# Performance work log

Measured on AMD Instinct MI355X. Metric: run time of the kernel, lower is better.

Reference implementation:

```python
import jax, jax.numpy as jnp
import numpy as np

Q_DIM = 1024
CTX_DIM = 1024
HEADS = 16
DIM_HEAD = 64
INNER = HEADS * DIM_HEAD  # 1024
MLP_HIDDEN = int(4.0 * Q_DIM)
EPS = 1e-5


def layer_norm(x, g, b):
    mu = jnp.mean(x, axis=-1, keepdims=True)
    var = jnp.var(x, axis=-1, keepdims=True)
    return (x - mu) * jax.lax.rsqrt(var + EPS) * g + b


def setup_inputs() -> dict:
    key = jax.random.key(0)
    ks = jax.random.split(key, 12)
    s = 0.02
    return {
        "x": jax.random.normal(ks[0], (4, 2048, Q_DIM), jnp.float32),
        "context": jax.random.normal(ks[1], (4, 2048, CTX_DIM), jnp.float32),
        # attention projections (stored [in, out])
        "Wq": jax.random.normal(ks[2], (Q_DIM, INNER), jnp.float32) * s,
        "Wk": jax.random.normal(ks[3], (CTX_DIM, INNER), jnp.float32) * s,
        "Wv": jax.random.normal(ks[4], (CTX_DIM, INNER), jnp.float32) * s,
        "Wo": jax.random.normal(ks[5], (INNER, Q_DIM), jnp.float32) * s,
        "bo": jnp.zeros((Q_DIM,), jnp.float32),
        # layer norms
        "g_q": jnp.ones((Q_DIM,), jnp.float32), "b_q": jnp.zeros((Q_DIM,), jnp.float32),
        "g_k": jnp.ones((CTX_DIM,), jnp.float32), "b_k": jnp.zeros((CTX_DIM,), jnp.float32),
        "g_m": jnp.ones((Q_DIM,), jnp.float32), "b_m": jnp.zeros((Q_DIM,), jnp.float32),
        # mlp
        "W1": jax.random.normal(ks[6], (Q_DIM, MLP_HIDDEN), jnp.float32) * s,
        "b1": jnp.zeros((MLP_HIDDEN,), jnp.float32),
        "W2": jax.random.normal(ks[7], (MLP_HIDDEN, Q_DIM), jnp.float32) * s,
        "b2": jnp.zeros((Q_DIM,), jnp.float32),
    }


def reference(x, context, Wq, Wk, Wv, Wo, bo, g_q, b_q, g_k, b_k, g_m, b_m, W1, b1, W2, b2):
    B, N, _ = x.shape
    M = context.shape[1]
    scale = DIM_HEAD ** -0.5

    xn = layer_norm(x, g_q, b_q)
    cn = layer_norm(context, g_k, b_k)

    # project and split heads: [B, H, N, D]
    q = (xn @ Wq).reshape(B, N, HEADS, DIM_HEAD).transpose(0, 2, 1, 3)
    k = (cn @ Wk).reshape(B, M, HEADS, DIM_HEAD).transpose(0, 2, 1, 3)
    v = (cn @ Wv).reshape(B, M, HEADS, DIM_HEAD).transpose(0, 2, 1, 3)

    sim = jnp.einsum('bhid,bhjd->bhij', q, k) * scale  # [B,H,N,M]
    attn = jax.nn.softmax(sim, axis=-1)
    out = jnp.einsum('bhij,bhjd->bhid', attn, v)        # [B,H,N,D]
    out = out.transpose(0, 2, 1, 3).reshape(B, N, INNER)
    x = x + out @ Wo + bo

    h = layer_norm(x, g_m, b_m)
    h = jax.nn.silu(h @ W1 + b1) @ W2 + b2
    return x + h
```

## Files before the change

kernel.cpp:

```cpp
#include <hip/hip_runtime.h>
#include <hip/hip_bf16.h>


typedef __bf16 bf16x8 __attribute__((ext_vector_type(8)));
typedef __bf16 bf16x4 __attribute__((ext_vector_type(4)));
typedef float f32x4 __attribute__((ext_vector_type(4)));

#define DEV static __device__ __forceinline__

DEV short f2bf(float x) {
  union { float f; unsigned u; } c; c.f = x;
  unsigned r = c.u + 0x7fffu + ((c.u >> 16) & 1u);
  return (short)(r >> 16);
}

DEV void gload_lds16(const void* g, void* l) {
  __builtin_amdgcn_global_load_lds((__attribute__((address_space(1))) void*)g,
                                   (__attribute__((address_space(3))) void*)l, 16, 0, 0);
}

__launch_bounds__(256, 4)
__global__ void transpose_f32_bf16(const float* __restrict__ in, short* __restrict__ outT,
                                   int R, int C) {
  __shared__ float t[32][33];
  const int c0 = blockIdx.x * 32, r0 = blockIdx.y * 32;
  const int tx = threadIdx.x, ty = threadIdx.y;
#pragma unroll
  for (int i = 0; i < 4; ++i)
    t[ty + 8 * i][tx] = in[(size_t)(r0 + ty + 8 * i) * C + (c0 + tx)];
  __syncthreads();
#pragma unroll
  for (int i = 0; i < 4; ++i)
    outT[(size_t)(c0 + ty + 8 * i) * R + (r0 + tx)] = f2bf(t[tx][ty + 8 * i]);
}

__launch_bounds__(256, 4)
__global__ void transpose_v(const short* __restrict__ V, short* __restrict__ Vt) {
  __shared__ short t[32][33];
  const int m0 = blockIdx.x * 32;
  const int d0 = blockIdx.y * 32;
  const int bh = blockIdx.z;
  const int b = bh >> 4, h = bh & 15;
  const int tx = threadIdx.x, ty = threadIdx.y;
#pragma unroll
  for (int i = 0; i < 4; ++i)
    t[ty + 8 * i][tx] = V[((size_t)b * 2048 + m0 + ty + 8 * i) * 1024 + h * 64 + d0 + tx];
  __syncthreads();
#pragma unroll
  for (int i = 0; i < 4; ++i)
    Vt[((size_t)bh * 64 + d0 + ty + 8 * i) * 2048 + (m0 + tx)] = t[tx][ty + 8 * i];
}

__launch_bounds__(256, 4)
__global__ void ln_kernel(const float* __restrict__ in, const float* __restrict__ g,
                          const float* __restrict__ b, short* __restrict__ out) {
  const int row = blockIdx.x;
  const int tid = threadIdx.x;
  const float4 v = ((const float4*)(in + (size_t)row * 1024))[tid];
  float s = v.x + v.y + v.z + v.w;
  float s2 = v.x * v.x + v.y * v.y + v.z * v.z + v.w * v.w;
#pragma unroll
  for (int off = 1; off < 64; off <<= 1) {
    s += __shfl_xor(s, off);
    s2 += __shfl_xor(s2, off);
  }
  __shared__ float ps[4], pq[4];
  const int w = tid >> 6, lane = tid & 63;
  if (lane == 0) { ps[w] = s; pq[w] = s2; }
  __syncthreads();
  s = ps[0] + ps[1] + ps[2] + ps[3];
  s2 = pq[0] + pq[1] + pq[2] + pq[3];
  const float mu = s * (1.f / 1024.f);
  const float rs = rsqrtf(s2 * (1.f / 1024.f) - mu * mu + 1e-5f);
  const float4 gg = ((const float4*)g)[tid];
  const float4 bb = ((const float4*)b)[tid];
  short4 o4;
  o4.x = f2bf((v.x - mu) * rs * gg.x + bb.x);
  o4.y = f2bf((v.y - mu) * rs * gg.y + bb.y);
  o4.z = f2bf((v.z - mu) * rs * gg.z + bb.z);
  o4.w = f2bf((v.w - mu) * rs * gg.w + bb.w);
  ((short4*)(out + (size_t)row * 1024))[tid] = o4;
}

enum { EPI_Q = 0, EPI_PLAIN = 1, EPI_BIAS_RESID_F32 = 2, EPI_BIAS_SILU = 3 };

template <int EPI>
__launch_bounds__(256, 2)
__global__ void gemm_bt(const short* __restrict__ A, const short* __restrict__ Bt,
                        int N, int K, const float* __restrict__ bias,
                        const float* __restrict__ resid, float scale,
                        short* __restrict__ outb, float* __restrict__ outf) {
  __shared__ short Al[128 * 64];
  __shared__ short Bl[128 * 64];
  const int tid = threadIdx.x;
  const int lane = tid & 63, w = tid >> 6;
  const int wrow = w >> 1, wcol = w & 1;
  const int lg = lane >> 4, lr = lane & 15;
  const int row0 = blockIdx.y * 128, col0 = blockIdx.x * 128;

  f32x4 acc[4][4] = {};

  const int sr = w * 32 + (lane >> 3);
  const int scb = ((lane & 7) * 16) ^ (((lane >> 3) & 7) << 4);
  const int fswz = (lr & 7) << 4;

  for (int kk = 0; kk < K; kk += 64) {
    __syncthreads();
#pragma unroll
    for (int i = 0; i < 4; ++i) {
      const int r = sr + i * 8;
      gload_lds16((const char*)(A + (size_t)(row0 + r) * K + kk) + scb,
                  (char*)Al + (size_t)(w * 32 + i * 8) * 128);
      gload_lds16((const char*)(Bt + (size_t)(col0 + r) * K + kk) + scb,
                  (char*)Bl + (size_t)(w * 32 + i * 8) * 128);
    }
    __syncthreads();
#pragma unroll
    for (int ks = 0; ks < 2; ++ks) {
      bf16x8 af[4], bfr[4];
#pragma unroll
      for (int mi = 0; mi < 4; ++mi) {
        const int r = wrow * 64 + mi * 16 + lr;
        af[mi] = *(const bf16x8*)((const char*)Al + r * 128 + ((ks * 64 + lg * 16) ^ fswz));
      }
#pragma unroll
      for (int ni = 0; ni < 4; ++ni) {
        const int c = wcol * 64 + ni * 16 + lr;
        bfr[ni] = *(const bf16x8*)((const char*)Bl + c * 128 + ((ks * 64 + lg * 16) ^ fswz));
      }
#pragma unroll
      for (int mi = 0; mi < 4; ++mi)
#pragma unroll
        for (int ni = 0; ni < 4; ++ni)
          acc[mi][ni] = __builtin_amdgcn_mfma_f32_16x16x32_bf16(af[mi], bfr[ni], acc[mi][ni], 0, 0, 0);
    }
  }
#pragma unroll
  for (int mi = 0; mi < 4; ++mi) {
#pragma unroll
    for (int ni = 0; ni < 4; ++ni) {
      const int cg = col0 + wcol * 64 + ni * 16 + lr;
#pragma unroll
      for (int r = 0; r < 4; ++r) {
        const int rg = row0 + wrow * 64 + mi * 16 + lg * 4 + r;
        const size_t idx = (size_t)rg * N + cg;
        const float v = acc[mi][ni][r];
        if constexpr (EPI == EPI_Q) {
          outb[idx] = f2bf(v * scale);
        } else if constexpr (EPI == EPI_PLAIN) {
          outb[idx] = f2bf(v);
        } else if constexpr (EPI == EPI_BIAS_RESID_F32) {
          outf[idx] = v + bias[cg] + resid[idx];
        } else {
          const float u = v + bias[cg];
          outb[idx] = f2bf(u / (1.f + __expf(-u)));
        }
      }
    }
  }
}

__launch_bounds__(512, 4)
__global__ void attn_kernel(const short* __restrict__ Qg, const short* __restrict__ Kg,
                            const short* __restrict__ Vtg, short* __restrict__ AO) {
  __shared__ short Kl[2][64 * 64];
  __shared__ short Vl[2][64 * 64];
  __shared__ short Pl[8][32 * 64];
  const int tid = threadIdx.x;
  const int lane = tid & 63, w = tid >> 6;
  const int lg = lane >> 4, lr = lane & 15;

  const int id = blockIdx.x;
  const int xcd = id & 7, j = id >> 3;
  const int bh = xcd * 8 + (j & 7);
  const int qblk = j >> 3;
  const int b = bh >> 4, h = bh & 15;
  const int q0 = qblk * 256 + w * 32;

  bf16x8 qf[2][2];
#pragma unroll
  for (int qb = 0; qb < 2; ++qb) {
    const short* qp = Qg + ((size_t)b * 2048 + q0 + qb * 16 + lr) * 1024 + h * 64 + lg * 8;
    qf[qb][0] = *(const bf16x8*)qp;
    qf[qb][1] = *(const bf16x8*)(qp + 32);
  }

  const int srow = lane >> 3;
  const int scb = ((lane & 7) << 4) ^ (srow << 4);
  const char* Ks = (const char*)Kg + ((size_t)b * 2048 + w * 8 + srow) * 2048 + h * 128 + scb;
  const char* Vs = (const char*)Vtg + ((size_t)bh * 64 + w * 8 + srow) * 4096 + scb;
  char* KB[2] = {(char*)&Kl[0][0] + w * 1024, (char*)&Kl[1][0] + w * 1024};
  char* VB[2] = {(char*)&Vl[0][0] + w * 1024, (char*)&Vl[1][0] + w * 1024};

  f32x4 acc[2][4] = {};
  float m_run[2] = {-1e30f, -1e30f};
  float l_run[2] = {0.f, 0.f};
  char* Pw = (char*)&Pl[w][0];
  const int sw = (lr & 7) << 4;

  gload_lds16(Ks, KB[0]);
  gload_lds16(Vs, VB[0]);
  __syncthreads();
  int buf = 0;

  for (int kv0 = 0; kv0 < 2048; kv0 += 64) {
    if (kv0 + 64 < 2048) {
      gload_lds16(Ks + (size_t)(kv0 + 64) * 2048, KB[buf ^ 1]);
      gload_lds16(Vs + (size_t)(kv0 + 64) * 2, VB[buf ^ 1]);
    }
    f32x4 st[4][2];
#pragma unroll
    for (int t = 0; t < 4; ++t) {
      const char* kb = (const char*)&Kl[buf][0] + (t * 16 + lr) * 128;
      const bf16x8 kf0 = *(const bf16x8*)(kb + ((lg * 16) ^ sw));
      const bf16x8 kf1 = *(const bf16x8*)(kb + ((64 + lg * 16) ^ sw));
#pragma unroll
      for (int qb = 0; qb < 2; ++qb) {
        f32x4 z = {};
        z = __builtin_amdgcn_mfma_f32_16x16x32_bf16(kf0, qf[qb][0], z, 0, 0, 0);
        z = __builtin_amdgcn_mfma_f32_16x16x32_bf16(kf1, qf[qb][1], z, 0, 0, 0);
        st[t][qb] = z;
      }
    }
#pragma unroll
    for (int qb = 0; qb < 2; ++qb) {
      float smax = st[0][qb][0];
#pragma unroll
      for (int t = 0; t < 4; ++t)
#pragma unroll
        for (int r = 0; r < 4; ++r) smax = fmaxf(smax, st[t][qb][r]);
      smax = fmaxf(smax, __shfl_xor(smax, 16));
      smax = fmaxf(smax, __shfl_xor(smax, 32));
      float m_use = m_run[qb];
      if (!__all(smax - m_use <= 8.f)) {
        const float mnew = fmaxf(m_use, smax);
        const float alpha = __builtin_amdgcn_exp2f(m_use - mnew);
        m_run[qb] = mnew;
        m_use = mnew;
        l_run[qb] *= alpha;
        float ar[4];
#pragma unroll
        for (int r = 0; r < 4; ++r) ar[r] = __shfl(alpha, lg * 4 + r);
#pragma unroll
        for (int dt = 0; dt < 4; ++dt)
#pragma unroll
          for (int r = 0; r < 4; ++r) acc[qb][dt][r] *= ar[r];
      }
      float rsum = 0.f;
#pragma unroll
      for (int t = 0; t < 4; ++t) {
        bf16x4 pk;
        float ps = 0.f;
#pragma unroll
        for (int r = 0; r < 4; ++r) {
          const float p = __builtin_amdgcn_exp2f(st[t][qb][r] - m_use);
          ps += p;
          pk[r] = (__bf16)p;
        }
        rsum += ps;
        *(bf16x4*)(Pw + (qb * 16 + lr) * 128 + ((t * 32 + lg * 8) ^ sw)) = pk;
      }
      rsum += __shfl_xor(rsum, 16);
      rsum += __shfl_xor(rsum, 32);
      l_run[qb] += rsum;
    }
#pragma unroll
    for (int c = 0; c < 2; ++c) {
      const bf16x8 pf0 = *(const bf16x8*)(Pw + lr * 128 + ((c * 64 + lg * 16) ^ sw));
      const bf16x8 pf1 = *(const bf16x8*)(Pw + (16 + lr) * 128 + ((c * 64 + lg * 16) ^ sw));
#pragma unroll
      for (int dt = 0; dt < 4; ++dt) {
        const bf16x8 vf = *(const bf16x8*)((const char*)&Vl[buf][0] + (dt * 16 + lr) * 128 +
                                           ((c * 64 + lg * 16) ^ sw));
        acc[0][dt] = __builtin_amdgcn_mfma_f32_16x16x32_bf16(pf0, vf, acc[0][dt], 0, 0, 0);
        acc[1][dt] = __builtin_amdgcn_mfma_f32_16x16x32_bf16(pf1, vf, acc[1][dt], 0, 0, 0);
      }
    }
    __syncthreads();
    buf ^= 1;
  }
#pragma unroll
  for (int qb = 0; qb < 2; ++qb) {
    const float linv = 1.f / l_run[qb];
    float lv[4];
#pragma unroll
    for (int r = 0; r < 4; ++r) lv[r] = __shfl(linv, lg * 4 + r);
#pragma unroll
    for (int dt = 0; dt < 4; ++dt)
#pragma unroll
      for (int r = 0; r < 4; ++r)
        AO[((size_t)b * 2048 + q0 + qb * 16 + lg * 4 + r) * 1024 + h * 64 + dt * 16 + lr] =
            f2bf(acc[qb][dt][r] * lv[r]);
  }
}

extern "C" void kernel_launch(void* const* d_in, const int* in_sizes, int n_in,
                              void* d_out, int out_size, void* d_ws, size_t ws_size,
                              hipStream_t stream) {
  const float* x   = (const float*)d_in[0];
  const float* ctx = (const float*)d_in[1];
  const float* Wq  = (const float*)d_in[2];
  const float* Wk  = (const float*)d_in[3];
  const float* Wv  = (const float*)d_in[4];
  const float* Wo  = (const float*)d_in[5];
  const float* bo  = (const float*)d_in[6];
  const float* g_q = (const float*)d_in[7];
  const float* b_q = (const float*)d_in[8];
  const float* g_k = (const float*)d_in[9];
  const float* b_k = (const float*)d_in[10];
  const float* g_m = (const float*)d_in[11];
  const float* b_m = (const float*)d_in[12];
  const float* W1  = (const float*)d_in[13];
  const float* b1  = (const float*)d_in[14];
  const float* W2  = (const float*)d_in[15];
  const float* b2  = (const float*)d_in[16];
  float* out = (float*)d_out;

  short* p = (short*)d_ws;
  short* xn  = p; p += (size_t)8192 * 1024;
  short* cn  = p; p += (size_t)8192 * 1024;
  short* Qb  = p; p += (size_t)8192 * 1024;
  short* Kb  = p; p += (size_t)8192 * 1024;
  short* Vb  = p; p += (size_t)8192 * 1024;
  short* Vts = p; p += (size_t)8192 * 1024;
  short* AO  = p; p += (size_t)8192 * 1024;
  short* hn  = p; p += (size_t)8192 * 1024;
  short* hm  = p; p += (size_t)8192 * 4096;
  short* WqT = p; p += (size_t)1024 * 1024;
  short* WkT = p; p += (size_t)1024 * 1024;
  short* WvT = p; p += (size_t)1024 * 1024;
  short* WoT = p; p += (size_t)1024 * 1024;
  short* W1T = p; p += (size_t)1024 * 4096;
  short* W2T = p; p += (size_t)4096 * 1024;
  float* x2  = (float*)p;

  const dim3 tb(32, 8);
  transpose_f32_bf16<<<dim3(32, 32), tb, 0, stream>>>(Wq, WqT, 1024, 1024);
  transpose_f32_bf16<<<dim3(32, 32), tb, 0, stream>>>(Wk, WkT, 1024, 1024);
  transpose_f32_bf16<<<dim3(32, 32), tb, 0, stream>>>(Wv, WvT, 1024, 1024);
  transpose_f32_bf16<<<dim3(32, 32), tb, 0, stream>>>(Wo, WoT, 1024, 1024);
  transpose_f32_bf16<<<dim3(128, 32), tb, 0, stream>>>(W1, W1T, 1024, 4096);
  transpose_f32_bf16<<<dim3(32, 128), tb, 0, stream>>>(W2, W2T, 4096, 1024);

  ln_kernel<<<8192, 256, 0, stream>>>(x, g_q, b_q, xn);
  ln_kernel<<<8192, 256, 0, stream>>>(ctx, g_k, b_k, cn);

  const float qscale = 0.125f * 1.44269504088896340736f;
  gemm_bt<EPI_Q><<<dim3(8, 64), 256, 0, stream>>>(xn, WqT, 1024, 1024, nullptr, nullptr, qscale, Qb, nullptr);
  gemm_bt<EPI_PLAIN><<<dim3(8, 64), 256, 0, stream>>>(cn, WkT, 1024, 1024, nullptr, nullptr, 0.f, Kb, nullptr);
  gemm_bt<EPI_PLAIN><<<dim3(8, 64), 256, 0, stream>>>(cn, WvT, 1024, 1024, nullptr, nullptr, 0.f, Vb, nullptr);

  transpose_v<<<dim3(64, 2, 64), tb, 0, stream>>>(Vb, Vts);

  attn_kernel<<<512, 512, 0, stream>>>(Qb, Kb, Vts, AO);

  gemm_bt<EPI_BIAS_RESID_F32><<<dim3(8, 64), 256, 0, stream>>>(AO, WoT, 1024, 1024, bo, x, 0.f, nullptr, x2);

  ln_kernel<<<8192, 256, 0, stream>>>(x2, g_m, b_m, hn);

  gemm_bt<EPI_BIAS_SILU><<<dim3(32, 64), 256, 0, stream>>>(hn, W1T, 4096, 1024, b1, nullptr, 0.f, hm, nullptr);
  gemm_bt<EPI_BIAS_RESID_F32><<<dim3(8, 64), 256, 0, stream>>>(hm, W2T, 1024, 4096, b2, x2, 0.f, nullptr, out);
}
```

Baseline: 459.3 us.

## Double-buffer GEMM LDS loads, add XCD-aware tile swizzle and 256x256 MLP GEMM

The GEMM main loop now double-buffers its A/B tiles in LDS and issues the next K-slice's async global-to-LDS loads in two halves, interleaved with MFMA work under explicit vmcnt waits and barriers. This hides global load latency behind compute. Workgroup IDs are remapped so consecutive tiles land on the same XCD for better L2 reuse, and the large W1 GEMM gets a new 256x256-tile, 512-thread variant. The cost is doubled LDS use, which lowers occupancy, plus more fragile hand-written waitcnt logic.

```diff
diff --git a/kernel.cpp b/kernel.cpp
--- a/kernel.cpp
+++ b/kernel.cpp
@@ -84,57 +84,226 @@
 
 enum { EPI_Q = 0, EPI_PLAIN = 1, EPI_BIAS_RESID_F32 = 2, EPI_BIAS_SILU = 3 };
 
+DEV void epi_store(int EPI, size_t idx, int cg, float v, const float* bias,
+                   const float* resid, float scale, short* outb, float* outf) {
+  if (EPI == EPI_Q) {
+    outb[idx] = f2bf(v * scale);
+  } else if (EPI == EPI_PLAIN) {
+    outb[idx] = f2bf(v);
+  } else if (EPI == EPI_BIAS_RESID_F32) {
+    outf[idx] = v + bias[cg] + resid[idx];
+  } else {
+    const float u = v + bias[cg];
+    outb[idx] = f2bf(u / (1.f + __expf(-u)));
+  }
+}
+
+template <int EPI>
+__launch_bounds__(512, 2)
+__global__ void gemm256(const short* __restrict__ A, const short* __restrict__ Bt,
+                        int N, int K, int nbx, const float* __restrict__ bias,
+                        const float* __restrict__ resid, float scale,
+                        short* __restrict__ outb, float* __restrict__ outf) {
+  __shared__ short Al[2][256 * 64];
+  __shared__ short Bl[2][256 * 64];
+  const int tid = threadIdx.x;
+  const int lane = tid & 63, w = tid >> 6;
+  const int wrow = w >> 2, wcol = w & 3;
+  const int lg = lane >> 4, lr = lane & 15;
+
+  const int nwg = gridDim.x;
+  const int id = blockIdx.x;
+  const int swz = (id & 7) * (nwg >> 3) + (id >> 3);
+  const int bx = swz % nbx, by = swz / nbx;
+  const int row0 = by * 256, col0 = bx * 256;
+
+  const size_t AROW = (size_t)K * 2;
+  const int srow8 = lane >> 3;
+  const int scb = ((lane & 7) << 4) ^ (srow8 << 4);
+  const char* Asrc = (const char*)A + (size_t)(row0 + w * 8 + srow8) * AROW + scb;
+  const char* Bsrc = (const char*)Bt + (size_t)(col0 + w * 8 + srow8) * AROW + scb;
+  const int ldst = (w * 8) * 128;
+  const int rsw = (lr & 7) << 4;
+  const int KT = K >> 6;
+
+#define ISS_A(i, kt, b) gload_lds16(Asrc + (size_t)((i) * 64) * AROW + (size_t)(kt) * 128, \
+                                    (char*)&Al[b][0] + ((i) * 64) * 128 + ldst)
+#define ISS_B(i, kt, b) gload_lds16(Bsrc + (size_t)((i) * 64) * AROW + (size_t)(kt) * 128, \
+                                    (char*)&Bl[b][0] + ((i) * 64) * 128 + ldst)
+
+  ISS_A(0, 0, 0); ISS_A(2, 0, 0); ISS_B(0, 0, 0); ISS_B(1, 0, 0);
+  ISS_B(2, 0, 0); ISS_B(3, 0, 0); ISS_A(1, 0, 0); ISS_A(3, 0, 0);
+
+  f32x4 acc[8][4] = {};
+  int bufc = 0;
+  for (int kt = 0; kt < KT; ++kt) {
+    const bool pref = (kt + 1 < KT);
+    const int nb = bufc ^ 1;
+    bf16x8 af[4][2], bfr[4][2];
+    __builtin_amdgcn_sched_barrier(0);
+    asm volatile("s_waitcnt vmcnt(2)" ::: "memory");
+    __builtin_amdgcn_s_barrier();
+    __builtin_amdgcn_sched_barrier(0);
+    if (pref) { ISS_A(0, kt + 1, nb); ISS_A(2, kt + 1, nb); ISS_B(0, kt + 1, nb); ISS_B(1, kt + 1, nb); }
+#pragma unroll
+    for (int ni = 0; ni < 4; ++ni) {
+      const int r = wcol * 64 + ni * 16 + lr;
+#pragma unroll
+      for (int ks = 0; ks < 2; ++ks)
+        bfr[ni][ks] = *(const bf16x8*)((const char*)&Bl[bufc][0] + r * 128 + ((ks * 64 + lg * 16) ^ rsw));
+    }
+#pragma unroll
+    for (int mq = 0; mq < 4; ++mq) {
+      const int r = wrow * 128 + mq * 16 + lr;
+#pragma unroll
+      for (int ks = 0; ks < 2; ++ks)
+        af[mq][ks] = *(const bf16x8*)((const char*)&Al[bufc][0] + r * 128 + ((ks * 64 + lg * 16) ^ rsw));
+    }
+    __builtin_amdgcn_s_setprio(1);
+#pragma unroll
+    for (int mq = 0; mq < 4; ++mq)
+#pragma unroll
+      for (int ni = 0; ni < 4; ++ni)
+#pragma unroll
+        for (int ks = 0; ks < 2; ++ks)
+          acc[mq][ni] = __builtin_amdgcn_mfma_f32_16x16x32_bf16(af[mq][ks], bfr[ni][ks], acc[mq][ni], 0, 0, 0);
+    __builtin_amdgcn_s_setprio(0);
+    __builtin_amdgcn_sched_barrier(0);
+    if (pref) asm volatile("s_waitcnt vmcnt(4)" ::: "memory");
+    else      asm volatile("s_waitcnt vmcnt(0)" ::: "memory");
+    __builtin_amdgcn_s_barrier();
+    __builtin_amdgcn_sched_barrier(0);
+    if (pref) { ISS_B(2, kt + 1, nb); ISS_B(3, kt + 1, nb); ISS_A(1, kt + 1, nb); ISS_A(3, kt + 1, nb); }
+#pragma unroll
+    for (int mq = 0; mq < 4; ++mq) {
+      const int r = wrow * 128 + 64 + mq * 16 + lr;
+#pragma unroll
+      for (int ks = 0; ks < 2; ++ks)
+        af[mq][ks] = *(const bf16x8*)((const char*)&Al[bufc][0] + r * 128 + ((ks * 64 + lg * 16) ^ rsw));
+    }
+    __builtin_amdgcn_s_setprio(1);
+#pragma unroll
+    for (int mq = 0; mq < 4; ++mq)
+#pragma unroll
+      for (int ni = 0; ni < 4; ++ni)
+#pragma unroll
+        for (int ks = 0; ks < 2; ++ks)
+          acc[4 + mq][ni] = __builtin_amdgcn_mfma_f32_16x16x32_bf16(af[mq][ks], bfr[ni][ks], acc[4 + mq][ni], 0, 0, 0);
+    __builtin_amdgcn_s_setprio(0);
+    bufc ^= 1;
+  }
+#undef ISS_A
+#undef ISS_B
+#pragma unroll
+  for (int mi = 0; mi < 8; ++mi) {
+#pragma unroll
+    for (int ni = 0; ni < 4; ++ni) {
+      const int cg = col0 + wcol * 64 + ni * 16 + lr;
+#pragma unroll
+      for (int r = 0; r < 4; ++r) {
+        const int rg = row0 + wrow * 128 + mi * 16 + lg * 4 + r;
+        epi_store(EPI, (size_t)rg * N + cg, cg, acc[mi][ni][r], bias, resid, scale, outb, outf);
+      }
+    }
+  }
+}
+
 template <int EPI>
 __launch_bounds__(256, 2)
-__global__ void gemm_bt(const short* __restrict__ A, const short* __restrict__ Bt,
-                        int N, int K, const float* __restrict__ bias,
+__global__ void gemm128(const short* __restrict__ A, const short* __restrict__ Bt,
+                        int N, int K, int nbx, const float* __restrict__ bias,
                         const float* __restrict__ resid, float scale,
                         short* __restrict__ outb, float* __restrict__ outf) {
-  __shared__ short Al[128 * 64];
-  __shared__ short Bl[128 * 64];
+  __shared__ short Al[2][128 * 64];
+  __shared__ short Bl[2][128 * 64];
   const int tid = threadIdx.x;
   const int lane = tid & 63, w = tid >> 6;
   const int wrow = w >> 1, wcol = w & 1;
   const int lg = lane >> 4, lr = lane & 15;
-  const int row0 = blockIdx.y * 128, col0 = blockIdx.x * 128;
+
+  const int nwg = gridDim.x;
+  const int id = blockIdx.x;
+  const int swz = (id & 7) * (nwg >> 3) + (id >> 3);
+  const int bx = swz % nbx, by = swz / nbx;
+  const int row0 = by * 128, col0 = bx * 128;
+
+  const size_t AROW = (size_t)K * 2;
+  const int srow8 = lane >> 3;
+  const int scb = ((lane & 7) << 4) ^ (srow8 << 4);
+  const char* Asrc = (const char*)A + (size_t)(row0 + w * 8 + srow8) * AROW + scb;
+  const char* Bsrc = (const char*)Bt + (size_t)(col0 + w * 8 + srow8) * AROW + scb;
+  const int ldst = (w * 8) * 128;
+  const int rsw = (lr & 7) << 4;
+  const int KT = K >> 6;
+
+#define ISS_A(i, kt, b) gload_lds16(Asrc + (size_t)((i) * 32) * AROW + (size_t)(kt) * 128, \
+                                    (char*)&Al[b][0] + ((i) * 32) * 128 + ldst)
+#define ISS_B(i, kt, b) gload_lds16(Bsrc + (size_t)((i) * 32) * AROW + (size_t)(kt) * 128, \
+                                    (char*)&Bl[b][0] + ((i) * 32) * 128 + ldst)
+
+  ISS_A(0, 0, 0); ISS_A(2, 0, 0); ISS_B(0, 0, 0); ISS_B(1, 0, 0);
+  ISS_B(2, 0, 0); ISS_B(3, 0, 0); ISS_A(1, 0, 0); ISS_A(3, 0, 0);
 
   f32x4 acc[4][4] = {};
-
-  const int sr = w * 32 + (lane >> 3);
-  const int scb = ((lane & 7) * 16) ^ (((lane >> 3) & 7) << 4);
-  const int fswz = (lr & 7) << 4;
-
-  for (int kk = 0; kk < K; kk += 64) {
-    __syncthreads();
-#pragma unroll
-    for (int i = 0; i < 4; ++i) {
-      const int r = sr + i * 8;
-      gload_lds16((const char*)(A + (size_t)(row0 + r) * K + kk) + scb,
-                  (char*)Al + (size_t)(w * 32 + i * 8) * 128);
-      gload_lds16((const char*)(Bt + (size_t)(col0 + r) * K + kk) + scb,
-                  (char*)Bl + (size_t)(w * 32 + i * 8) * 128);
-    }
-    __syncthreads();
-#pragma unroll
-    for (int ks = 0; ks < 2; ++ks) {
-      bf16x8 af[4], bfr[4];
-#pragma unroll
-      for (int mi = 0; mi < 4; ++mi) {
-        const int r = wrow * 64 + mi * 16 + lr;
-        af[mi] = *(const bf16x8*)((const char*)Al + r * 128 + ((ks * 64 + lg * 16) ^ fswz));
-      }
-#pragma unroll
-      for (int ni = 0; ni < 4; ++ni) {
-        const int c = wcol * 64 + ni * 16 + lr;
-        bfr[ni] = *(const bf16x8*)((const char*)Bl + c * 128 + ((ks * 64 + lg * 16) ^ fswz));
-      }
-#pragma unroll
-      for (int mi = 0; mi < 4; ++mi)
-#pragma unroll
-        for (int ni = 0; ni < 4; ++ni)
-          acc[mi][ni] = __builtin_amdgcn_mfma_f32_16x16x32_bf16(af[mi], bfr[ni], acc[mi][ni], 0, 0, 0);
-    }
-  }
+  int bufc = 0;
+  for (int kt = 0; kt < KT; ++kt) {
+    const bool pref = (kt + 1 < KT);
+    const int nb = bufc ^ 1;
+    bf16x8 af[2][2], bfr[4][2];
+    __builtin_amdgcn_sched_barrier(0);
+    asm volatile("s_waitcnt vmcnt(2)" ::: "memory");
+    __builtin_amdgcn_s_barrier();
+    __builtin_amdgcn_sched_barrier(0);
+    if (pref) { ISS_A(0, kt + 1, nb); ISS_A(2, kt + 1, nb); ISS_B(0, kt + 1, nb); ISS_B(1, kt + 1, nb); }
+#pragma unroll
+    for (int ni = 0; ni < 4; ++ni) {
+      const int r = wcol * 64 + ni * 16 + lr;
+#pragma unroll
+      for (int ks = 0; ks < 2; ++ks)
+        bfr[ni][ks] = *(const bf16x8*)((const char*)&Bl[bufc][0] + r * 128 + ((ks * 64 + lg * 16) ^ rsw));
+    }
+#pragma unroll
+    for (int mq = 0; mq < 2; ++mq) {
+      const int r = wrow * 64 + mq * 16 + lr;
+#pragma unroll
+      for (int ks = 0; ks < 2; ++ks)
+        af[mq][ks] = *(const bf16x8*)((const char*)&Al[bufc][0] + r * 128 + ((ks * 64 + lg * 16) ^ rsw));
+    }
+    __builtin_amdgcn_s_setprio(1);
+#pragma unroll
+    for (int mq = 0; mq < 2; ++mq)
+#pragma unroll
+      for (int ni = 0; ni < 4; ++ni)
+#pragma unroll
+        for (int ks = 0; ks < 2; ++ks)
+          acc[mq][ni] = __builtin_amdgcn_mfma_f32_16x16x32_bf16(af[mq][ks], bfr[ni][ks], acc[mq][ni], 0, 0, 0);
+    __builtin_amdgcn_s_setprio(0);
+    __builtin_amdgcn_sched_barrier(0);
+    if (pref) asm volatile("s_waitcnt vmcnt(4)" ::: "memory");
+    else      asm volatile("s_waitcnt vmcnt(0)" ::: "memory");
+    __builtin_amdgcn_s_barrier();
+    __builtin_amdgcn_sched_barrier(0);
+    if (pref) { ISS_B(2, kt + 1, nb); ISS_B(3, kt + 1, nb); ISS_A(1, kt + 1, nb); ISS_A(3, kt + 1, nb); }
+#pragma unroll
+    for (int mq = 0; mq < 2; ++mq) {
+      const int r = wrow * 64 + 32 + mq * 16 + lr;
+#pragma unroll
+      for (int ks = 0; ks < 2; ++ks)
+        af[mq][ks] = *(const bf16x8*)((const char*)&Al[bufc][0] + r * 128 + ((ks * 64 + lg * 16) ^ rsw));
+    }
+    __builtin_amdgcn_s_setprio(1);
+#pragma unroll
+    for (int mq = 0; mq < 2; ++mq)
+#pragma unroll
+      for (int ni = 0; ni < 4; ++ni)
+#pragma unroll
+        for (int ks = 0; ks < 2; ++ks)
+          acc[2 + mq][ni] = __builtin_amdgcn_mfma_f32_16x16x32_bf16(af[mq][ks], bfr[ni][ks], acc[2 + mq][ni], 0, 0, 0);
+    __builtin_amdgcn_s_setprio(0);
+    bufc ^= 1;
+  }
+#undef ISS_A
+#undef ISS_B
 #pragma unroll
   for (int mi = 0; mi < 4; ++mi) {
 #pragma unroll
@@ -143,18 +312,7 @@
 #pragma unroll
       for (int r = 0; r < 4; ++r) {
         const int rg = row0 + wrow * 64 + mi * 16 + lg * 4 + r;
-        const size_t idx = (size_t)rg * N + cg;
-        const float v = acc[mi][ni][r];
-        if constexpr (EPI == EPI_Q) {
-          outb[idx] = f2bf(v * scale);
-        } else if constexpr (EPI == EPI_PLAIN) {
-          outb[idx] = f2bf(v);
-        } else if constexpr (EPI == EPI_BIAS_RESID_F32) {
-          outf[idx] = v + bias[cg] + resid[idx];
-        } else {
-          const float u = v + bias[cg];
-          outb[idx] = f2bf(u / (1.f + __expf(-u)));
-        }
+        epi_store(EPI, (size_t)rg * N + cg, cg, acc[mi][ni][r], bias, resid, scale, outb, outf);
       }
     }
   }
@@ -346,18 +504,18 @@
   ln_kernel<<<8192, 256, 0, stream>>>(ctx, g_k, b_k, cn);
 
   const float qscale = 0.125f * 1.44269504088896340736f;
-  gemm_bt<EPI_Q><<<dim3(8, 64), 256, 0, stream>>>(xn, WqT, 1024, 1024, nullptr, nullptr, qscale, Qb, nullptr);
-  gemm_bt<EPI_PLAIN><<<dim3(8, 64), 256, 0, stream>>>(cn, WkT, 1024, 1024, nullptr, nullptr, 0.f, Kb, nullptr);
-  gemm_bt<EPI_PLAIN><<<dim3(8, 64), 256, 0, stream>>>(cn, WvT, 1024, 1024, nullptr, nullptr, 0.f, Vb, nullptr);
+  gemm128<EPI_Q><<<512, 256, 0, stream>>>(xn, WqT, 1024, 1024, 8, nullptr, nullptr, qscale, Qb, nullptr);
+  gemm128<EPI_PLAIN><<<512, 256, 0, stream>>>(cn, WkT, 1024, 1024, 8, nullptr, nullptr, 0.f, Kb, nullptr);
+  gemm128<EPI_PLAIN><<<512, 256, 0, stream>>>(cn, WvT, 1024, 1024, 8, nullptr, nullptr, 0.f, Vb, nullptr);
 
   transpose_v<<<dim3(64, 2, 64), tb, 0, stream>>>(Vb, Vts);
 
   attn_kernel<<<512, 512, 0, stream>>>(Qb, Kb, Vts, AO);
 
-  gemm_bt<EPI_BIAS_RESID_F32><<<dim3(8, 64), 256, 0, stream>>>(AO, WoT, 1024, 1024, bo, x, 0.f, nullptr, x2);
+  gemm128<EPI_BIAS_RESID_F32><<<512, 256, 0, stream>>>(AO, WoT, 1024, 1024, 8, bo, x, 0.f, nullptr, x2);
 
   ln_kernel<<<8192, 256, 0, stream>>>(x2, g_m, b_m, hn);
 
-  gemm_bt<EPI_BIAS_SILU><<<dim3(32, 64), 256, 0, stream>>>(hn, W1T, 4096, 1024, b1, nullptr, 0.f, hm, nullptr);
-  gemm_bt<EPI_BIAS_RESID_F32><<<dim3(8, 64), 256, 0, stream>>>(hm, W2T, 1024, 4096, b2, x2, 0.f, nullptr, out);
-}
+  gemm256<EPI_BIAS_SILU><<<512, 512, 0, stream>>>(hn, W1T, 4096, 1024, 16, b1, nullptr, 0.f, hm, nullptr);
+  gemm128<EPI_BIAS_RESID_F32><<<512, 256, 0, stream>>>(hm, W2T, 1024, 4096, 8, b2, x2, 0.f, nullptr, out);
+}
```

Measured after the change: 496.1 us. +8.0%, slower.

## Replace GEMMs with 256x256 pipelined kernel, fuse K/V projection, split-K for W2

Applied to the files above, without the earlier changes.

Replaces the 128x128 single-buffered GEMM with a 256x256-tile, 512-thread kernel. It double-buffers LDS with direct global-to-LDS loads, splits each tile into phases with explicit waitcnt and barriers, raises MFMA priority, and swizzles block IDs across XCDs. The K and V projections are merged into one GEMM against a concatenated weight, and the attention and V-transpose kernels are re-strided to read the interleaved KV buffer. The final W2 GEMM uses 2-way split-K into fp32 partials held in the reused Q buffer, followed by a separate reduce kernel that adds bias and residual. The goal is more data reuse per tile and better overlap of loads with MFMA, paid for with larger LDS use, fewer blocks in flight, and extra partial-sum traffic.

```diff
diff --git a/kernel.cpp b/kernel.cpp
--- a/kernel.cpp
+++ b/kernel.cpp
@@ -35,7 +35,7 @@
 }
 
 __launch_bounds__(256, 4)
-__global__ void transpose_v(const short* __restrict__ V, short* __restrict__ Vt) {
+__global__ void transpose_v(const short* __restrict__ KV, short* __restrict__ Vt) {
   __shared__ short t[32][33];
   const int m0 = blockIdx.x * 32;
   const int d0 = blockIdx.y * 32;
@@ -44,7 +44,7 @@
   const int tx = threadIdx.x, ty = threadIdx.y;
 #pragma unroll
   for (int i = 0; i < 4; ++i)
-    t[ty + 8 * i][tx] = V[((size_t)b * 2048 + m0 + ty + 8 * i) * 1024 + h * 64 + d0 + tx];
+    t[ty + 8 * i][tx] = KV[((size_t)b * 2048 + m0 + ty + 8 * i) * 2048 + 1024 + h * 64 + d0 + tx];
   __syncthreads();
 #pragma unroll
   for (int i = 0; i < 4; ++i)
@@ -82,86 +82,186 @@
   ((short4*)(out + (size_t)row * 1024))[tid] = o4;
 }
 
-enum { EPI_Q = 0, EPI_PLAIN = 1, EPI_BIAS_RESID_F32 = 2, EPI_BIAS_SILU = 3 };
+enum { EPI_Q = 0, EPI_PLAIN = 1, EPI_BIAS_RESID_F32 = 2, EPI_BIAS_SILU = 3, EPI_PARTIAL = 4 };
+
+DEV void epi_store(int EPI, size_t idx, int cg, float v, const float* bias,
+                   const float* resid, float scale, short* outb, float* outf) {
+  if (EPI == EPI_Q) {
+    outb[idx] = f2bf(v * scale);
+  } else if (EPI == EPI_PLAIN) {
+    outb[idx] = f2bf(v);
+  } else if (EPI == EPI_BIAS_RESID_F32) {
+    outf[idx] = v + bias[cg] + resid[idx];
+  } else if (EPI == EPI_BIAS_SILU) {
+    const float u = v + bias[cg];
+    outb[idx] = f2bf(u / (1.f + __expf(-u)));
+  } else {
+    outf[idx] = v;
+  }
+}
 
 template <int EPI>
-__launch_bounds__(256, 2)
-__global__ void gemm_bt(const short* __restrict__ A, const short* __restrict__ Bt,
-                        int N, int K, const float* __restrict__ bias,
-                        const float* __restrict__ resid, float scale,
-                        short* __restrict__ outb, float* __restrict__ outf) {
-  __shared__ short Al[128 * 64];
-  __shared__ short Bl[128 * 64];
+DEV void gemm_core(const short* __restrict__ A, const short* __restrict__ Bt,
+                   int lda, int ldb, int k0, int nit, int N, int nbx, int nwg, int id,
+                   const float* __restrict__ bias, const float* __restrict__ resid,
+                   float scale, short* __restrict__ outb, float* __restrict__ outf,
+                   char* Albase, char* Blbase) {
   const int tid = threadIdx.x;
   const int lane = tid & 63, w = tid >> 6;
-  const int wrow = w >> 1, wcol = w & 1;
+  const int wr = w >> 2, wc = w & 3;
   const int lg = lane >> 4, lr = lane & 15;
-  const int row0 = blockIdx.y * 128, col0 = blockIdx.x * 128;
-
-  f32x4 acc[4][4] = {};
-
-  const int sr = w * 32 + (lane >> 3);
-  const int scb = ((lane & 7) * 16) ^ (((lane >> 3) & 7) << 4);
-  const int fswz = (lr & 7) << 4;
-
-  for (int kk = 0; kk < K; kk += 64) {
-    __syncthreads();
-#pragma unroll
-    for (int i = 0; i < 4; ++i) {
-      const int r = sr + i * 8;
-      gload_lds16((const char*)(A + (size_t)(row0 + r) * K + kk) + scb,
-                  (char*)Al + (size_t)(w * 32 + i * 8) * 128);
-      gload_lds16((const char*)(Bt + (size_t)(col0 + r) * K + kk) + scb,
-                  (char*)Bl + (size_t)(w * 32 + i * 8) * 128);
-    }
-    __syncthreads();
-#pragma unroll
-    for (int ks = 0; ks < 2; ++ks) {
-      bf16x8 af[4], bfr[4];
-#pragma unroll
-      for (int mi = 0; mi < 4; ++mi) {
-        const int r = wrow * 64 + mi * 16 + lr;
-        af[mi] = *(const bf16x8*)((const char*)Al + r * 128 + ((ks * 64 + lg * 16) ^ fswz));
-      }
-#pragma unroll
-      for (int ni = 0; ni < 4; ++ni) {
-        const int c = wcol * 64 + ni * 16 + lr;
-        bfr[ni] = *(const bf16x8*)((const char*)Bl + c * 128 + ((ks * 64 + lg * 16) ^ fswz));
-      }
-#pragma unroll
-      for (int mi = 0; mi < 4; ++mi)
-#pragma unroll
-        for (int ni = 0; ni < 4; ++ni)
-          acc[mi][ni] = __builtin_amdgcn_mfma_f32_16x16x32_bf16(af[mi], bfr[ni], acc[mi][ni], 0, 0, 0);
-    }
-  }
-#pragma unroll
-  for (int mi = 0; mi < 4; ++mi) {
-#pragma unroll
-    for (int ni = 0; ni < 4; ++ni) {
-      const int cg = col0 + wcol * 64 + ni * 16 + lr;
+  const int swz = (id & 7) * (nwg >> 3) + (id >> 3);
+  const int bx = swz % nbx, by = swz / nbx;
+  const int row0 = by * 256, col0 = bx * 256;
+  const int rsw = (lr & 7) << 4;
+  const int scb = (((tid & 7) ^ ((tid >> 3) & 7)) << 4);
+  const size_t lda2 = (size_t)lda * 2, ldb2 = (size_t)ldb * 2;
+  const char* Asrc = (const char*)A + (size_t)(row0 + (tid >> 3)) * lda2 + (size_t)k0 * 2 + scb;
+  const char* Bsrc = (const char*)Bt + (size_t)(col0 + (tid >> 3)) * ldb2 + (size_t)k0 * 2 + scb;
+  char* Adst = Albase + w * 1024;
+  char* Bdst = Blbase + w * 1024;
+
+#define STG_A(t, h) do { \
+    gload_lds16(Asrc + (size_t)((h) * 128) * lda2 + (size_t)(t) * 128, \
+                Adst + (((t) & 1) * 2 + (h)) * 16384); \
+    gload_lds16(Asrc + (size_t)((h) * 128 + 64) * lda2 + (size_t)(t) * 128, \
+                Adst + (((t) & 1) * 2 + (h)) * 16384 + 8192); } while (0)
+#define STG_B(t, h) do { \
+    gload_lds16(Bsrc + (size_t)((h) * 128) * ldb2 + (size_t)(t) * 128, \
+                Bdst + (((t) & 1) * 2 + (h)) * 16384); \
+    gload_lds16(Bsrc + (size_t)((h) * 128 + 64) * ldb2 + (size_t)(t) * 128, \
+                Bdst + (((t) & 1) * 2 + (h)) * 16384 + 8192); } while (0)
+#define RD_A(buf, mq, mi, ks) (*(const bf16x8*)(Albase + ((buf) * 2 + wr) * 16384 + \
+    ((mq) * 64 + (mi) * 16 + lr) * 128 + (((ks) * 64 + lg * 16) ^ rsw)))
+#define RD_B(buf, nq, ni, ks) (*(const bf16x8*)(Blbase + ((buf) * 2 + (wc >> 1)) * 16384 + \
+    ((wc & 1) * 64 + (nq) * 32 + (ni) * 16 + lr) * 128 + (((ks) * 64 + lg * 16) ^ rsw)))
+#define MFMA_Q(mq, nq, BF) do { \
+    __builtin_amdgcn_s_setprio(1); \
+    _Pragma("unroll") for (int mi_ = 0; mi_ < 4; ++mi_) \
+    _Pragma("unroll") for (int ni_ = 0; ni_ < 2; ++ni_) \
+    _Pragma("unroll") for (int ks_ = 0; ks_ < 2; ++ks_) \
+      acc[(mq) * 4 + mi_][(nq) * 2 + ni_] = __builtin_amdgcn_mfma_f32_16x16x32_bf16( \
+          af[mi_][ks_], BF[ni_][ks_], acc[(mq) * 4 + mi_][(nq) * 2 + ni_], 0, 0, 0); \
+    __builtin_amdgcn_s_setprio(0); } while (0)
+#define PH_ENTRY() do { __builtin_amdgcn_sched_barrier(0); __builtin_amdgcn_s_barrier(); \
+    __builtin_amdgcn_sched_barrier(0); } while (0)
+#define PH_LGKM() do { asm volatile("s_waitcnt lgkmcnt(0)" ::: "memory"); \
+    __builtin_amdgcn_sched_barrier(0); } while (0)
+
+  STG_B(0, 0); STG_B(0, 1); STG_A(0, 0); STG_A(0, 1);
+  STG_B(1, 0); STG_B(1, 1); STG_A(1, 0); STG_A(1, 1);
+
+  f32x4 acc[8][4] = {};
+  bf16x8 af[4][2], b0[2][2], b1[2][2];
+
+#pragma unroll 1
+  for (int i = 0; i < nit; ++i) {
+    const int t2 = 2 * i + 2, t3 = 2 * i + 3;
+    const bool pf = (i + 1 < nit);
+    asm volatile("s_waitcnt vmcnt(8)" ::: "memory");
+    PH_ENTRY();
+#pragma unroll
+    for (int mi = 0; mi < 4; ++mi) { af[mi][0] = RD_A(0, 0, mi, 0); af[mi][1] = RD_A(0, 0, mi, 1); }
+#pragma unroll
+    for (int ni = 0; ni < 2; ++ni) { b0[ni][0] = RD_B(0, 0, ni, 0); b0[ni][1] = RD_B(0, 0, ni, 1); }
+    PH_LGKM();
+    MFMA_Q(0, 0, b0);
+    PH_ENTRY();
+#pragma unroll
+    for (int ni = 0; ni < 2; ++ni) { b1[ni][0] = RD_B(0, 1, ni, 0); b1[ni][1] = RD_B(0, 1, ni, 1); }
+    PH_LGKM();
+    MFMA_Q(0, 1, b1);
+    PH_ENTRY();
+#pragma unroll
+    for (int mi = 0; mi < 4; ++mi) { af[mi][0] = RD_A(0, 1, mi, 0); af[mi][1] = RD_A(0, 1, mi, 1); }
+    if (pf) { STG_B(t2, 0); STG_B(t2, 1); }
+    PH_LGKM();
+    MFMA_Q(1, 0, b0);
+    PH_ENTRY();
+    if (pf) { STG_A(t2, 0); STG_A(t2, 1); }
+    PH_LGKM();
+    MFMA_Q(1, 1, b1);
+    if (pf) asm volatile("s_waitcnt vmcnt(8)" ::: "memory");
+    else    asm volatile("s_waitcnt vmcnt(0)" ::: "memory");
+    PH_ENTRY();
+#pragma unroll
+    for (int mi = 0; mi < 4; ++mi) { af[mi][0] = RD_A(1, 0, mi, 0); af[mi][1] = RD_A(1, 0, mi, 1); }
+#pragma unroll
+    for (int ni = 0; ni < 2; ++ni) { b0[ni][0] = RD_B(1, 0, ni, 0); b0[ni][1] = RD_B(1, 0, ni, 1); }
+    PH_LGKM();
+    MFMA_Q(0, 0, b0);
+    PH_ENTRY();
+#pragma unroll
+    for (int ni = 0; ni < 2; ++ni) { b1[ni][0] = RD_B(1, 1, ni, 0); b1[ni][1] = RD_B(1, 1, ni, 1); }
+    PH_LGKM();
+    MFMA_Q(0, 1, b1);
+    PH_ENTRY();
+#pragma unroll
+    for (int mi = 0; mi < 4; ++mi) { af[mi][0] = RD_A(1, 1, mi, 0); af[mi][1] = RD_A(1, 1, mi, 1); }
+    if (pf) { STG_B(t3, 0); STG_B(t3, 1); }
+    PH_LGKM();
+    MFMA_Q(1, 0, b0);
+    PH_ENTRY();
+    if (pf) { STG_A(t3, 0); STG_A(t3, 1); }
+    PH_LGKM();
+    MFMA_Q(1, 1, b1);
+  }
+#undef STG_A
+#undef STG_B
+#undef RD_A
+#undef RD_B
+#undef MFMA_Q
+#undef PH_ENTRY
+#undef PH_LGKM
+#pragma unroll
+  for (int mi = 0; mi < 8; ++mi) {
+#pragma unroll
+    for (int nj = 0; nj < 4; ++nj) {
+      const int cg = col0 + wc * 64 + (nj >> 1) * 32 + (nj & 1) * 16 + lr;
 #pragma unroll
       for (int r = 0; r < 4; ++r) {
-        const int rg = row0 + wrow * 64 + mi * 16 + lg * 4 + r;
-        const size_t idx = (size_t)rg * N + cg;
-        const float v = acc[mi][ni][r];
-        if constexpr (EPI == EPI_Q) {
-          outb[idx] = f2bf(v * scale);
-        } else if constexpr (EPI == EPI_PLAIN) {
-          outb[idx] = f2bf(v);
-        } else if constexpr (EPI == EPI_BIAS_RESID_F32) {
-          outf[idx] = v + bias[cg] + resid[idx];
-        } else {
-          const float u = v + bias[cg];
-          outb[idx] = f2bf(u / (1.f + __expf(-u)));
-        }
+        const int rg = row0 + wr * 128 + (mi >> 2) * 64 + (mi & 3) * 16 + lg * 4 + r;
+        epi_store(EPI, (size_t)rg * N + cg, cg, acc[mi][nj][r], bias, resid, scale, outb, outf);
       }
     }
   }
 }
 
+template <int EPI>
+__launch_bounds__(512, 2)
+__global__ void gemm256k(const short* __restrict__ A, const short* __restrict__ Bt,
+                         int lda, int ldb, int ksub, int N, int nbx,
+                         const float* __restrict__ bias, const float* __restrict__ resid,
+                         float scale, short* __restrict__ outb, float* __restrict__ outf) {
+  __shared__ short Al[2][2][128 * 64];
+  __shared__ short Bl[2][2][128 * 64];
+  const int k0 = blockIdx.y * ksub;
+  float* of = outf;
+  if (EPI == EPI_PARTIAL) of = outf + (size_t)blockIdx.y * 8192 * 1024;
+  gemm_core<EPI>(A, Bt, lda, ldb, k0, ksub >> 7, N, nbx, gridDim.x, blockIdx.x,
+                 bias, resid, scale, outb, of, (char*)&Al[0][0][0], (char*)&Bl[0][0][0]);
+}
+
+__launch_bounds__(256, 8)
+__global__ void splitk_reduce(const float* __restrict__ p0, const float* __restrict__ p1,
+                              const float* __restrict__ bias, const float* __restrict__ resid,
+                              float* __restrict__ out) {
+  const size_t i = (size_t)blockIdx.x * 256 + threadIdx.x;
+  const int col4 = (int)(i & 255);
+  const float4 a = ((const float4*)p0)[i];
+  const float4 b = ((const float4*)p1)[i];
+  const float4 c = ((const float4*)resid)[i];
+  const float4 g = ((const float4*)bias)[col4];
+  float4 o;
+  o.x = a.x + b.x + c.x + g.x;
+  o.y = a.y + b.y + c.y + g.y;
+  o.z = a.z + b.z + c.z + g.z;
+  o.w = a.w + b.w + c.w + g.w;
+  ((float4*)out)[i] = o;
+}
+
 __launch_bounds__(512, 4)
-__global__ void attn_kernel(const short* __restrict__ Qg, const short* __restrict__ Kg,
+__global__ void attn_kernel(const short* __restrict__ Qg, const short* __restrict__ KVg,
                             const short* __restrict__ Vtg, short* __restrict__ AO) {
   __shared__ short Kl[2][64 * 64];
   __shared__ short Vl[2][64 * 64];
@@ -187,7 +287,7 @@
 
   const int srow = lane >> 3;
   const int scb = ((lane & 7) << 4) ^ (srow << 4);
-  const char* Ks = (const char*)Kg + ((size_t)b * 2048 + w * 8 + srow) * 2048 + h * 128 + scb;
+  const char* Ks = (const char*)KVg + ((size_t)b * 2048 + w * 8 + srow) * 4096 + h * 128 + scb;
   const char* Vs = (const char*)Vtg + ((size_t)bh * 64 + w * 8 + srow) * 4096 + scb;
   char* KB[2] = {(char*)&Kl[0][0] + w * 1024, (char*)&Kl[1][0] + w * 1024};
   char* VB[2] = {(char*)&Vl[0][0] + w * 1024, (char*)&Vl[1][0] + w * 1024};
@@ -205,7 +305,7 @@
 
   for (int kv0 = 0; kv0 < 2048; kv0 += 64) {
     if (kv0 + 64 < 2048) {
-      gload_lds16(Ks + (size_t)(kv0 + 64) * 2048, KB[buf ^ 1]);
+      gload_lds16(Ks + (size_t)(kv0 + 64) * 4096, KB[buf ^ 1]);
       gload_lds16(Vs + (size_t)(kv0 + 64) * 2, VB[buf ^ 1]);
     }
     f32x4 st[4][2];
@@ -317,27 +417,26 @@
   float* out = (float*)d_out;
 
   short* p = (short*)d_ws;
-  short* xn  = p; p += (size_t)8192 * 1024;
-  short* cn  = p; p += (size_t)8192 * 1024;
-  short* Qb  = p; p += (size_t)8192 * 1024;
-  short* Kb  = p; p += (size_t)8192 * 1024;
-  short* Vb  = p; p += (size_t)8192 * 1024;
-  short* Vts = p; p += (size_t)8192 * 1024;
-  short* AO  = p; p += (size_t)8192 * 1024;
-  short* hn  = p; p += (size_t)8192 * 1024;
-  short* hm  = p; p += (size_t)8192 * 4096;
-  short* WqT = p; p += (size_t)1024 * 1024;
-  short* WkT = p; p += (size_t)1024 * 1024;
-  short* WvT = p; p += (size_t)1024 * 1024;
-  short* WoT = p; p += (size_t)1024 * 1024;
-  short* W1T = p; p += (size_t)1024 * 4096;
-  short* W2T = p; p += (size_t)4096 * 1024;
-  float* x2  = (float*)p;
+  short* xn   = p; p += (size_t)8192 * 1024;
+  short* cn   = p; p += (size_t)8192 * 1024;
+  short* Qb   = p; p += (size_t)8192 * 1024;
+  short* KVb  = p; p += (size_t)8192 * 2048;
+  short* Vts  = p; p += (size_t)8192 * 1024;
+  short* AO   = p; p += (size_t)8192 * 1024;
+  short* hn   = p; p += (size_t)8192 * 1024;
+  short* hm   = p; p += (size_t)8192 * 4096;
+  short* WqT  = p; p += (size_t)1024 * 1024;
+  short* WkvT = p; p += (size_t)2048 * 1024;
+  short* WoT  = p; p += (size_t)1024 * 1024;
+  short* W1T  = p; p += (size_t)1024 * 4096;
+  short* W2T  = p; p += (size_t)4096 * 1024;
+  float* x2   = (float*)p;
+  float* part = (float*)Qb;
 
   const dim3 tb(32, 8);
   transpose_f32_bf16<<<dim3(32, 32), tb, 0, stream>>>(Wq, WqT, 1024, 1024);
-  transpose_f32_bf16<<<dim3(32, 32), tb, 0, stream>>>(Wk, WkT, 1024, 1024);
-  transpose_f32_bf16<<<dim3(32, 32), tb, 0, stream>>>(Wv, WvT, 1024, 1024);
+  transpose_f32_bf16<<<dim3(32, 32), tb, 0, stream>>>(Wk, WkvT, 1024, 1024);
+  transpose_f32_bf16<<<dim3(32, 32), tb, 0, stream>>>(Wv, WkvT + (size_t)1024 * 1024, 1024, 1024);
   transpose_f32_bf16<<<dim3(32, 32), tb, 0, stream>>>(Wo, WoT, 1024, 1024);
   transpose_f32_bf16<<<dim3(128, 32), tb, 0, stream>>>(W1, W1T, 1024, 4096);
   transpose_f32_bf16<<<dim3(32, 128), tb, 0, stream>>>(W2, W2T, 4096, 1024);
@@ -346,18 +445,23 @@
   ln_kernel<<<8192, 256, 0, stream>>>(ctx, g_k, b_k, cn);
 
   const float qscale = 0.125f * 1.44269504088896340736f;
-  gemm_bt<EPI_Q><<<dim3(8, 64), 256, 0, stream>>>(xn, WqT, 1024, 1024, nullptr, nullptr, qscale, Qb, nullptr);
-  gemm_bt<EPI_PLAIN><<<dim3(8, 64), 256, 0, stream>>>(cn, WkT, 1024, 1024, nullptr, nullptr, 0.f, Kb, nullptr);
-  gemm_bt<EPI_PLAIN><<<dim3(8, 64), 256, 0, stream>>>(cn, WvT, 1024, 1024, nullptr, nullptr, 0.f, Vb, nullptr);
-
-  transpose_v<<<dim3(64, 2, 64), tb, 0, stream>>>(Vb, Vts);
-
-  attn_kernel<<<512, 512, 0, stream>>>(Qb, Kb, Vts, AO);
-
-  gemm_bt<EPI_BIAS_RESID_F32><<<dim3(8, 64), 256, 0, stream>>>(AO, WoT, 1024, 1024, bo, x, 0.f, nullptr, x2);
+  gemm256k<EPI_Q><<<dim3(128, 1), 512, 0, stream>>>(xn, WqT, 1024, 1024, 1024, 1024, 4,
+                                                    nullptr, nullptr, qscale, Qb, nullptr);
+  gemm256k<EPI_PLAIN><<<dim3(256, 1), 512, 0, stream>>>(cn, WkvT, 1024, 1024, 1024, 2048, 8,
+                                                        nullptr, nullptr, 0.f, KVb, nullptr);
+
+  transpose_v<<<dim3(64, 2, 64), tb, 0, stream>>>(KVb, Vts);
+
+  attn_kernel<<<512, 512, 0, stream>>>(Qb, KVb, Vts, AO);
+
+  gemm256k<EPI_BIAS_RESID_F32><<<dim3(128, 1), 512, 0, stream>>>(AO, WoT, 1024, 1024, 1024, 1024, 4,
+                                                                 bo, x, 0.f, nullptr, x2);
 
   ln_kernel<<<8192, 256, 0, stream>>>(x2, g_m, b_m, hn);
 
-  gemm_bt<EPI_BIAS_SILU><<<dim3(32, 64), 256, 0, stream>>>(hn, W1T, 4096, 1024, b1, nullptr, 0.f, hm, nullptr);
-  gemm_bt<EPI_BIAS_RESID_F32><<<dim3(8, 64), 256, 0, stream>>>(hm, W2T, 1024, 4096, b2, x2, 0.f, nullptr, out);
-}
+  gemm256k<EPI_BIAS_SILU><<<dim3(512, 1), 512, 0, stream>>>(hn, W1T, 1024, 1024, 1024, 4096, 16,
+                                                            b1, nullptr, 0.f, hm, nullptr);
+  gemm256k<EPI_PARTIAL><<<dim3(128, 2), 512, 0, stream>>>(hm, W2T, 4096, 4096, 2048, 1024, 4,
+                                                          nullptr, nullptr, 0.f, nullptr, part);
+  splitk_reduce<<<8192, 256, 0, stream>>>(part, part + (size_t)8192 * 1024, b2, x2, out);
+}
```

Measured after the change: 432.5 us. 1.06x faster.

## Fuse K and V projections into one GEMM and swizzle GEMM blocks across XCDs

Applied to the files above, without the earlier changes.

Concatenates the transposed Wk and Wv into a single weight so K and V come from one GEMM writing an interleaved KV buffer. The attention and V-transpose kernels are updated to read this combined layout with the doubled row stride. Separately, every GEMM now runs on a 1D grid and remaps block ids so consecutive tiles land on the same XCD, aiming for better L2 reuse. The fused GEMM reads the context activations once instead of twice, but the strided KV layout may cost some locality in attention.

```diff
diff --git a/kernel.cpp b/kernel.cpp
--- a/kernel.cpp
+++ b/kernel.cpp
@@ -35,7 +35,7 @@
 }
 
 __launch_bounds__(256, 4)
-__global__ void transpose_v(const short* __restrict__ V, short* __restrict__ Vt) {
+__global__ void transpose_v(const short* __restrict__ KV, short* __restrict__ Vt) {
   __shared__ short t[32][33];
   const int m0 = blockIdx.x * 32;
   const int d0 = blockIdx.y * 32;
@@ -44,7 +44,7 @@
   const int tx = threadIdx.x, ty = threadIdx.y;
 #pragma unroll
   for (int i = 0; i < 4; ++i)
-    t[ty + 8 * i][tx] = V[((size_t)b * 2048 + m0 + ty + 8 * i) * 1024 + h * 64 + d0 + tx];
+    t[ty + 8 * i][tx] = KV[((size_t)b * 2048 + m0 + ty + 8 * i) * 2048 + 1024 + h * 64 + d0 + tx];
   __syncthreads();
 #pragma unroll
   for (int i = 0; i < 4; ++i)
@@ -87,7 +87,7 @@
 template <int EPI>
 __launch_bounds__(256, 2)
 __global__ void gemm_bt(const short* __restrict__ A, const short* __restrict__ Bt,
-                        int N, int K, const float* __restrict__ bias,
+                        int N, int K, int nbx, const float* __restrict__ bias,
                         const float* __restrict__ resid, float scale,
                         short* __restrict__ outb, float* __restrict__ outf) {
   __shared__ short Al[128 * 64];
@@ -96,7 +96,11 @@
   const int lane = tid & 63, w = tid >> 6;
   const int wrow = w >> 1, wcol = w & 1;
   const int lg = lane >> 4, lr = lane & 15;
-  const int row0 = blockIdx.y * 128, col0 = blockIdx.x * 128;
+
+  const int nwg = gridDim.x, id = blockIdx.x;
+  const int swz = (id & 7) * (nwg >> 3) + (id >> 3);
+  const int bx = swz % nbx, by = swz / nbx;
+  const int row0 = by * 128, col0 = bx * 128;
 
   f32x4 acc[4][4] = {};
 
@@ -161,7 +165,7 @@
 }
 
 __launch_bounds__(512, 4)
-__global__ void attn_kernel(const short* __restrict__ Qg, const short* __restrict__ Kg,
+__global__ void attn_kernel(const short* __restrict__ Qg, const short* __restrict__ KVg,
                             const short* __restrict__ Vtg, short* __restrict__ AO) {
   __shared__ short Kl[2][64 * 64];
   __shared__ short Vl[2][64 * 64];
@@ -187,7 +191,7 @@
 
   const int srow = lane >> 3;
   const int scb = ((lane & 7) << 4) ^ (srow << 4);
-  const char* Ks = (const char*)Kg + ((size_t)b * 2048 + w * 8 + srow) * 2048 + h * 128 + scb;
+  const char* Ks = (const char*)KVg + ((size_t)b * 2048 + w * 8 + srow) * 4096 + h * 128 + scb;
   const char* Vs = (const char*)Vtg + ((size_t)bh * 64 + w * 8 + srow) * 4096 + scb;
   char* KB[2] = {(char*)&Kl[0][0] + w * 1024, (char*)&Kl[1][0] + w * 1024};
   char* VB[2] = {(char*)&Vl[0][0] + w * 1024, (char*)&Vl[1][0] + w * 1024};
@@ -205,7 +209,7 @@
 
   for (int kv0 = 0; kv0 < 2048; kv0 += 64) {
     if (kv0 + 64 < 2048) {
-      gload_lds16(Ks + (size_t)(kv0 + 64) * 2048, KB[buf ^ 1]);
+      gload_lds16(Ks + (size_t)(kv0 + 64) * 4096, KB[buf ^ 1]);
       gload_lds16(Vs + (size_t)(kv0 + 64) * 2, VB[buf ^ 1]);
     }
     f32x4 st[4][2];
@@ -317,27 +321,25 @@
   float* out = (float*)d_out;
 
   short* p = (short*)d_ws;
-  short* xn  = p; p += (size_t)8192 * 1024;
-  short* cn  = p; p += (size_t)8192 * 1024;
-  short* Qb  = p; p += (size_t)8192 * 1024;
-  short* Kb  = p; p += (size_t)8192 * 1024;
-  short* Vb  = p; p += (size_t)8192 * 1024;
-  short* Vts = p; p += (size_t)8192 * 1024;
-  short* AO  = p; p += (size_t)8192 * 1024;
-  short* hn  = p; p += (size_t)8192 * 1024;
-  short* hm  = p; p += (size_t)8192 * 4096;
-  short* WqT = p; p += (size_t)1024 * 1024;
-  short* WkT = p; p += (size_t)1024 * 1024;
-  short* WvT = p; p += (size_t)1024 * 1024;
-  short* WoT = p; p += (size_t)1024 * 1024;
-  short* W1T = p; p += (size_t)1024 * 4096;
-  short* W2T = p; p += (size_t)4096 * 1024;
-  float* x2  = (float*)p;
+  short* xn   = p; p += (size_t)8192 * 1024;
+  short* cn   = p; p += (size_t)8192 * 1024;
+  short* Qb   = p; p += (size_t)8192 * 1024;
+  short* KVb  = p; p += (size_t)8192 * 2048;
+  short* Vts  = p; p += (size_t)8192 * 1024;
+  short* AO   = p; p += (size_t)8192 * 1024;
+  short* hn   = p; p += (size_t)8192 * 1024;
+  short* hm   = p; p += (size_t)8192 * 4096;
+  short* WqT  = p; p += (size_t)1024 * 1024;
+  short* WkvT = p; p += (size_t)2048 * 1024;
+  short* WoT  = p; p += (size_t)1024 * 1024;
+  short* W1T  = p; p += (size_t)1024 * 4096;
+  short* W2T  = p; p += (size_t)4096 * 1024;
+  float* x2   = (float*)p;
 
   const dim3 tb(32, 8);
   transpose_f32_bf16<<<dim3(32, 32), tb, 0, stream>>>(Wq, WqT, 1024, 1024);
-  transpose_f32_bf16<<<dim3(32, 32), tb, 0, stream>>>(Wk, WkT, 1024, 1024);
-  transpose_f32_bf16<<<dim3(32, 32), tb, 0, stream>>>(Wv, WvT, 1024, 1024);
+  transpose_f32_bf16<<<dim3(32, 32), tb, 0, stream>>>(Wk, WkvT, 1024, 1024);
+  transpose_f32_bf16<<<dim3(32, 32), tb, 0, stream>>>(Wv, WkvT + (size_t)1024 * 1024, 1024, 1024);
   transpose_f32_bf16<<<dim3(32, 32), tb, 0, stream>>>(Wo, WoT, 1024, 1024);
   transpose_f32_bf16<<<dim3(128, 32), tb, 0, stream>>>(W1, W1T, 1024, 4096);
   transpose_f32_bf16<<<dim3(32, 128), tb, 0, stream>>>(W2, W2T, 4096, 1024);
@@ -346,18 +348,17 @@
   ln_kernel<<<8192, 256, 0, stream>>>(ctx, g_k, b_k, cn);
 
   const float qscale = 0.125f * 1.44269504088896340736f;
-  gemm_bt<EPI_Q><<<dim3(8, 64), 256, 0, stream>>>(xn, WqT, 1024, 1024, nullptr, nullptr, qscale, Qb, nullptr);
-  gemm_bt<EPI_PLAIN><<<dim3(8, 64), 256, 0, stream>>>(cn, WkT, 1024, 1024, nullptr, nullptr, 0.f, Kb, nullptr);
-  gemm_bt<EPI_PLAIN><<<dim3(8, 64), 256, 0, stream>>>(cn, WvT, 1024, 1024, nullptr, nullptr, 0.f, Vb, nullptr);
-
-  transpose_v<<<dim3(64, 2, 64), tb, 0, stream>>>(Vb, Vts);
-
-  attn_kernel<<<512, 512, 0, stream>>>(Qb, Kb, Vts, AO);
-
-  gemm_bt<EPI_BIAS_RESID_F32><<<dim3(8, 64), 256, 0, stream>>>(AO, WoT, 1024, 1024, bo, x, 0.f, nullptr, x2);
+  gemm_bt<EPI_Q><<<512, 256, 0, stream>>>(xn, WqT, 1024, 1024, 8, nullptr, nullptr, qscale, Qb, nullptr);
+  gemm_bt<EPI_PLAIN><<<1024, 256, 0, stream>>>(cn, WkvT, 2048, 1024, 16, nullptr, nullptr, 0.f, KVb, nullptr);
+
+  transpose_v<<<dim3(64, 2, 64), tb, 0, stream>>>(KVb, Vts);
+
+  attn_kernel<<<512, 512, 0, stream>>>(Qb, KVb, Vts, AO);
+
+  gemm_bt<EPI_BIAS_RESID_F32><<<512, 256, 0, stream>>>(AO, WoT, 1024, 1024, 8, bo, x, 0.f, nullptr, x2);
 
   ln_kernel<<<8192, 256, 0, stream>>>(x2, g_m, b_m, hn);
 
-  gemm_bt<EPI_BIAS_SILU><<<dim3(32, 64), 256, 0, stream>>>(hn, W1T, 4096, 1024, b1, nullptr, 0.f, hm, nullptr);
-  gemm_bt<EPI_BIAS_RESID_F32><<<dim3(8, 64), 256, 0, stream>>>(hm, W2T, 1024, 4096, b2, x2, 0.f, nullptr, out);
-}
+  gemm_bt<EPI_BIAS_SILU><<<2048, 256, 0, stream>>>(hn, W1T, 4096, 1024, 32, b1, nullptr, 0.f, hm, nullptr);
+  gemm_bt<EPI_BIAS_RESID_F32><<<512, 256, 0, stream>>>(hm, W2T, 1024, 4096, 8, b2, x2, 0.f, nullptr, out);
+}
```

New measurement: 436.8 us. 4.9% less time.
